# Kernel optimization log

Measured on AMD Instinct MI355X. Metric: run time of the kernel, lower is better.

The kernel has to match this reference:

```python
import jax, jax.numpy as jnp
from jax import lax
import numpy as np

B, T, I, H, C = 32, 256, 128, 128, 100


def setup_inputs() -> dict:
    key = jax.random.key(0)
    ks = jax.random.split(key, 9)
    s = 1.0 / np.sqrt(H)  # PyTorch LSTMCell init range
    inp = {
        "x": jax.random.normal(ks[0], (B, T, I), dtype=jnp.float32),
        "w_ih": jax.random.uniform(ks[1], (4 * H, I), jnp.float32, -s, s),
        "b_ih": jax.random.uniform(ks[2], (4 * H,), jnp.float32, -s, s),
        "w_hh": jax.random.uniform(ks[3], (4 * H, H), jnp.float32, -s, s),
        "b_hh": jax.random.uniform(ks[4], (4 * H,), jnp.float32, -s, s),
        # attention params: normal(mean=0, std=0.01) per the source
        "w1": 0.01 * jax.random.normal(ks[5], (2 * H, H), dtype=jnp.float32),
        "w2": 0.01 * jax.random.normal(ks[6], (H, 1), dtype=jnp.float32),
        "w_fc": jax.random.uniform(ks[7], (C, H), jnp.float32, -s, s),
        "b_fc": jax.random.uniform(ks[8], (C,), jnp.float32, -s, s),
    }
    return inp


def _forward(x, w_ih, b_ih, w_hh, b_hh, w1, w2, w_fc, b_fc):
    Bv, Tv, _ = x.shape
    Hv = w_hh.shape[1]
    h0 = jnp.zeros((Bv, Hv), x.dtype)
    c0 = jnp.zeros((Bv, Hv), x.dtype)
    # memory buffer: slot 0 holds the initial zero hidden state (as in the
    # torch code, h_old starts as h_t=0); slots 1..T filled as we go.
    # Unwritten (future) slots are zero, so their attn contribution
    # attn_w * h_old is exactly zero -> no mask needed, matching the
    # growing-memory semantics of the original loop.
    mem0 = jnp.zeros((Bv, Tv + 1, Hv), x.dtype)
    attn0 = jnp.zeros((Bv, Hv), x.dtype)

    def step(carry, inp):
        h, c, mem, _ = carry
        x_t, i = inp
        # PyTorch LSTMCell: gate order i, f, g, o
        gates = x_t @ w_ih.T + b_ih + h @ w_hh.T + b_hh
        ig, fg, gg, og = jnp.split(gates, 4, axis=-1)
        c = jax.nn.sigmoid(fg) * c + jax.nn.sigmoid(ig) * jnp.tanh(gg)
        h = jax.nn.sigmoid(og) * jnp.tanh(c)
        # additive attention scores over the memory (NO softmax in source)
        h_rep = jnp.broadcast_to(h[:, None, :], mem.shape)  # [B, T+1, H]
        cat = jnp.concatenate([h_rep, mem], axis=-1)        # [B, T+1, 2H]
        s = jnp.tanh(cat @ w1) @ w2                          # [B, T+1, 1]
        attn_c = jnp.sum(s * mem, axis=1)                    # [B, H]
        mem = mem.at[:, i + 1, :].set(h)  # append h_t to memory
        return (h, c, mem, attn_c), None

    xs = (jnp.transpose(x, (1, 0, 2)), jnp.arange(Tv))
    (h, c, mem, attn_c), _ = lax.scan(step, (h0, c0, mem0, attn0), xs)
    return (h + attn_c) @ w_fc.T + b_fc


def reference(x, w_ih, b_ih, w_hh, b_hh, w1, w2, w_fc, b_fc):
    return _forward(x, w_ih, b_ih, w_hh, b_hh, w1, w2, w_fc, b_fc)
```

## Files before the change

kernel.cpp:

```cpp
#include <hip/hip_runtime.h>
#include <hip/hip_bf16.h>


#define Bsz 32
#define Tsz 256
#define Isz 128
#define Hsz 128
#define Csz 100
#define G4H 512

typedef short v8s __attribute__((ext_vector_type(8)));
typedef float v4fa __attribute__((ext_vector_type(4)));
typedef float v2f __attribute__((ext_vector_type(2)));

__device__ __forceinline__ v2f mk2(float a, float b) { v2f r; r.x = a; r.y = b; return r; }
__device__ __forceinline__ float quad_rsum(float x) {
    int t = __builtin_amdgcn_update_dpp(0, __float_as_int(x), 0xB1, 0xF, 0xF, true);
    x += __int_as_float(t);
    t = __builtin_amdgcn_update_dpp(0, __float_as_int(x), 0x4E, 0xF, 0xF, true);
    x += __int_as_float(t);
    return x;
}
__device__ __forceinline__ float rcpf(float x) { return __builtin_amdgcn_rcpf(x); }
__device__ __forceinline__ float ex2(float x) { return __builtin_amdgcn_exp2f(x); }
__device__ __forceinline__ float sigm_n(float x) {
    return rcpf(1.0f + ex2(-1.442695041f * x));
}
__device__ __forceinline__ float tanh_n(float x) {
    return fmaf(-2.0f, rcpf(1.0f + ex2(2.885390082f * x)), 1.0f);
}
__device__ __forceinline__ short bf16_bits(float x) {
    __hip_bfloat16 h = __float2bfloat16(x);
    return *reinterpret_cast<short*>(&h);
}
__device__ __forceinline__ float bf16_val(float x) {
    return __bfloat162float(__float2bfloat16(x));
}

__global__ __launch_bounds__(256) void prep_kernel(
    const float* __restrict__ w_ih, const float* __restrict__ b_ih,
    const float* __restrict__ w_hh, const float* __restrict__ b_hh,
    const float* __restrict__ w1,
    __hip_bfloat16* __restrict__ W2ih, __hip_bfloat16* __restrict__ W2v,
    float* __restrict__ whh_pk, float* __restrict__ bias,
    float* __restrict__ attn_c) {
    int idx = blockIdx.x * blockDim.x + threadIdx.x;
    if (idx < G4H * Isz) {
        int n = idx >> 7;
        int k = idx & 127;
        float x = w_ih[idx];
        __hip_bfloat16 hi = __float2bfloat16(x);
        __hip_bfloat16 lo = __float2bfloat16(x - __bfloat162float(hi));
        W2ih[(size_t)n * 384 + k] = hi;
        W2ih[(size_t)n * 384 + 128 + k] = lo;
        W2ih[(size_t)n * 384 + 256 + k] = hi;

        int j4  = idx & 3;
        int q   = (idx >> 2) & 3;
        int d   = (idx >> 4) & 127;
        int gi  = (idx >> 11) & 3;
        int kk4 = (idx >> 13) & 7;
        whh_pk[idx] = w_hh[(size_t)((gi << 7) + d) * 128 + (q << 5) + (kk4 << 2) + j4];
    }
    if (idx < Hsz * Hsz) {
        int n = idx >> 7;
        int k = idx & 127;
        float x = w1[(size_t)(128 + k) * Hsz + n];
        __hip_bfloat16 hi = __float2bfloat16(x);
        __hip_bfloat16 lo = __float2bfloat16(x - __bfloat162float(hi));
        W2v[(size_t)n * 384 + k] = hi;
        W2v[(size_t)n * 384 + 128 + k] = lo;
        W2v[(size_t)n * 384 + 256 + k] = hi;
    }
    if (idx < G4H) bias[idx] = b_ih[idx] + b_hh[idx];
    if (idx < Bsz * Hsz) attn_c[idx] = 0.0f;
}

__global__ __launch_bounds__(256) void gemm_mfma_f32a(
    const float* __restrict__ A, const __hip_bfloat16* __restrict__ W2,
    const float* __restrict__ bias, float* __restrict__ C, int M, int N) {
    const int tid = threadIdx.x;
    const int w = tid >> 6, lane = tid & 63;
    const int m0 = blockIdx.y * 64 + (w & 1) * 32;
    const int n0 = blockIdx.x * 64 + (w >> 1) * 32;
    const int r = lane & 15, quad = lane >> 4;

    v8s Ahi[2][4], Alo[2][4];
    #pragma unroll
    for (int i = 0; i < 2; ++i)
        #pragma unroll
        for (int cb = 0; cb < 4; ++cb) {
            const float* src = A + (size_t)(m0 + 16 * i + r) * Isz + cb * 32 + quad * 8;
            float4 f0 = *(const float4*)src;
            float4 f1 = *(const float4*)(src + 4);
            float f[8] = {f0.x, f0.y, f0.z, f0.w, f1.x, f1.y, f1.z, f1.w};
            v8s hi, lo;
            #pragma unroll
            for (int e = 0; e < 8; ++e) {
                float hv = bf16_val(f[e]);
                hi[e] = bf16_bits(f[e]);
                lo[e] = bf16_bits(f[e] - hv);
            }
            Ahi[i][cb] = hi;
            Alo[i][cb] = lo;
        }

    v4fa acc[2][2] = {};
    const short* Wb = (const short*)W2;
    #pragma unroll
    for (int ks = 0; ks < 12; ++ks) {
        int cb = ks & 3;
        v8s a0 = (ks >= 8) ? Alo[0][cb] : Ahi[0][cb];
        v8s a1 = (ks >= 8) ? Alo[1][cb] : Ahi[1][cb];
        int kb = ks * 32 + quad * 8;
        v8s b0 = *(const v8s*)(Wb + (size_t)(n0 + r) * 384 + kb);
        v8s b1 = *(const v8s*)(Wb + (size_t)(n0 + 16 + r) * 384 + kb);
        acc[0][0] = __builtin_amdgcn_mfma_f32_16x16x32_bf16(a0, b0, acc[0][0], 0, 0, 0);
        acc[0][1] = __builtin_amdgcn_mfma_f32_16x16x32_bf16(a0, b1, acc[0][1], 0, 0, 0);
        acc[1][0] = __builtin_amdgcn_mfma_f32_16x16x32_bf16(a1, b0, acc[1][0], 0, 0, 0);
        acc[1][1] = __builtin_amdgcn_mfma_f32_16x16x32_bf16(a1, b1, acc[1][1], 0, 0, 0);
    }
    #pragma unroll
    for (int i = 0; i < 2; ++i)
        #pragma unroll
        for (int j = 0; j < 2; ++j) {
            int cn = n0 + 16 * j + r;
            float bb = bias ? bias[cn] : 0.0f;
            #pragma unroll
            for (int rr = 0; rr < 4; ++rr) {
                int row = m0 + 16 * i + quad * 4 + rr;
                C[(size_t)row * N + cn] = acc[i][j][rr] + bb;
            }
        }
}

#define HPAD(k) ((k) + 8 * ((k) >> 5))

__global__ __launch_bounds__(512, 2) void lstm_seq(
    const float* __restrict__ G, const float* __restrict__ whh_pk,
    float* __restrict__ H_all) {
    const int b = blockIdx.x;
    const int tid = threadIdx.x;
    const int d = tid >> 2;
    const int q = tid & 3;

    __shared__ float h_s[2][160];

    v2f w2v[4][16];
    {
        const float4* wp = (const float4*)whh_pk;
        #pragma unroll
        for (int kk4 = 0; kk4 < 8; ++kk4)
            #pragma unroll
            for (int gi = 0; gi < 4; ++gi) {
                float4 v = wp[((kk4 * 4 + gi) * 128 + d) * 4 + q];
                w2v[gi][kk4 * 2]     = mk2(v.x, v.y);
                w2v[gi][kk4 * 2 + 1] = mk2(v.z, v.w);
            }
    }

    if (tid < 320) ((float*)h_s)[tid] = 0.0f;
    float c = 0.0f;
    __syncthreads();

    const float* Gq = G + (size_t)b * Tsz * G4H + q * 128 + d;
    float* Hst = H_all + (size_t)b * Tsz * Hsz + d;

    float gval = Gq[0];
    int cur = 0;
    for (int t = 0; t < Tsz; ++t) {
        const int tn = (t < Tsz - 1) ? t + 1 : t;
        float ngval = Gq[(size_t)tn * G4H];

        v2f accA[4], accB[4];
        #pragma unroll
        for (int gi = 0; gi < 4; ++gi) {
            accA[gi] = mk2(q == gi ? gval : 0.f, 0.f);
            accB[gi] = mk2(0.f, 0.f);
        }
        const float4* hb4 = (const float4*)&h_s[cur][q * 40];
        #pragma unroll
        for (int kk4 = 0; kk4 < 8; ++kk4) {
            float4 h4 = hb4[kk4];
            v2f hA = mk2(h4.x, h4.y);
            v2f hB = mk2(h4.z, h4.w);
            accA[0] = __builtin_elementwise_fma(hA, w2v[0][2 * kk4], accA[0]);
            accA[1] = __builtin_elementwise_fma(hA, w2v[1][2 * kk4], accA[1]);
            accA[2] = __builtin_elementwise_fma(hA, w2v[2][2 * kk4], accA[2]);
            accA[3] = __builtin_elementwise_fma(hA, w2v[3][2 * kk4], accA[3]);
            accB[0] = __builtin_elementwise_fma(hB, w2v[0][2 * kk4 + 1], accB[0]);
            accB[1] = __builtin_elementwise_fma(hB, w2v[1][2 * kk4 + 1], accB[1]);
            accB[2] = __builtin_elementwise_fma(hB, w2v[2][2 * kk4 + 1], accB[2]);
            accB[3] = __builtin_elementwise_fma(hB, w2v[3][2 * kk4 + 1], accB[3]);
        }
        float a0 = quad_rsum(accA[0].x + accA[0].y + accB[0].x + accB[0].y);
        float a1 = quad_rsum(accA[1].x + accA[1].y + accB[1].x + accB[1].y);
        float a2 = quad_rsum(accA[2].x + accA[2].y + accB[2].x + accB[2].y);
        float a3 = quad_rsum(accA[3].x + accA[3].y + accB[3].x + accB[3].y);

        float iv = sigm_n(a0);
        float fv = sigm_n(a1);
        float gv = tanh_n(a2);
        float ov = sigm_n(a3);
        c = fmaf(fv, c, iv * gv);
        float h = ov * tanh_n(c);

        if (q == 0) {
            h_s[cur ^ 1][HPAD(d)] = h;
            Hst[(size_t)t * Hsz] = h;
        }
        gval = ngval;
        __builtin_amdgcn_sched_barrier(0);
        asm volatile("s_waitcnt lgkmcnt(0)" ::: "memory");
        __builtin_amdgcn_s_barrier();
        __builtin_amdgcn_sched_barrier(0);
        cur ^= 1;
    }
}

__global__ __launch_bounds__(256) void kv_scores(
    const float* __restrict__ H_all, const __hip_bfloat16* __restrict__ W2v,
    const float* __restrict__ w1, const float* __restrict__ w2,
    float* __restrict__ attn_c) {
    const int b = blockIdx.x >> 2, jt = blockIdx.x & 3;
    const int tid = threadIdx.x;
    __shared__ float kv_s[64][132];
    __shared__ float hT[Hsz];
    __shared__ float q_s[Hsz];
    __shared__ float w2s[Hsz];
    __shared__ float s_s[64];
    __shared__ float part[2][Hsz];

    const float* Hb = H_all + (size_t)b * Tsz * Hsz;

    if (tid < Hsz) {
        hT[tid] = Hb[255 * Hsz + tid];
        w2s[tid] = w2[tid];
    }

    {
        const int w = tid >> 6, lane = tid & 63;
        const int m0 = (w & 1) * 32;
        const int n0 = (w >> 1) * 32;
        const int r = lane & 15, quad = lane >> 4;
        const float* Abase = Hb + (size_t)(jt * 64) * Hsz;

        v8s Ahi[2][4], Alo[2][4];
        #pragma unroll
        for (int i = 0; i < 2; ++i)
            #pragma unroll
            for (int cb = 0; cb < 4; ++cb) {
                const float* src = Abase + (size_t)(m0 + 16 * i + r) * Hsz + cb * 32 + quad * 8;
                float4 f0 = *(const float4*)src;
                float4 f1 = *(const float4*)(src + 4);
                float f[8] = {f0.x, f0.y, f0.z, f0.w, f1.x, f1.y, f1.z, f1.w};
                v8s hi, lo;
                #pragma unroll
                for (int e = 0; e < 8; ++e) {
                    float hv = bf16_val(f[e]);
                    hi[e] = bf16_bits(f[e]);
                    lo[e] = bf16_bits(f[e] - hv);
                }
                Ahi[i][cb] = hi;
                Alo[i][cb] = lo;
            }

        v4fa acc[2][2][2] = {};
        const short* Wb = (const short*)W2v;
        #pragma unroll
        for (int ks = 0; ks < 12; ++ks) {
            int cb = ks & 3;
            v8s a0 = (ks >= 8) ? Alo[0][cb] : Ahi[0][cb];
            v8s a1 = (ks >= 8) ? Alo[1][cb] : Ahi[1][cb];
            int kb = ks * 32 + quad * 8;
            #pragma unroll
            for (int nh = 0; nh < 2; ++nh) {
                int nn = nh * 64 + n0;
                v8s b0 = *(const v8s*)(Wb + (size_t)(nn + r) * 384 + kb);
                v8s b1 = *(const v8s*)(Wb + (size_t)(nn + 16 + r) * 384 + kb);
                acc[nh][0][0] = __builtin_amdgcn_mfma_f32_16x16x32_bf16(a0, b0, acc[nh][0][0], 0, 0, 0);
                acc[nh][0][1] = __builtin_amdgcn_mfma_f32_16x16x32_bf16(a0, b1, acc[nh][0][1], 0, 0, 0);
                acc[nh][1][0] = __builtin_amdgcn_mfma_f32_16x16x32_bf16(a1, b0, acc[nh][1][0], 0, 0, 0);
                acc[nh][1][1] = __builtin_amdgcn_mfma_f32_16x16x32_bf16(a1, b1, acc[nh][1][1], 0, 0, 0);
            }
        }
        #pragma unroll
        for (int nh = 0; nh < 2; ++nh)
            #pragma unroll
            for (int i = 0; i < 2; ++i)
                #pragma unroll
                for (int j = 0; j < 2; ++j)
                    #pragma unroll
                    for (int rr = 0; rr < 4; ++rr)
                        kv_s[m0 + 16 * i + quad * 4 + rr][nh * 64 + n0 + 16 * j + r] =
                            acc[nh][i][j][rr];
    }
    __syncthreads();

    if (tid < Hsz) {
        float acc = 0.f;
        #pragma unroll 8
        for (int k = 0; k < Hsz; ++k) acc = fmaf(hT[k], w1[k * Hsz + tid], acc);
        q_s[tid] = acc;
    }
    __syncthreads();

    const int jl = tid >> 2, ql = tid & 3;
    const int j = jt * 64 + jl;
    float p = 0.f;
    if (j < 255) {
        #pragma unroll 8
        for (int kk = 0; kk < 32; ++kk) {
            int k = ql * 32 + ((kk + ql) & 31);
            p = fmaf(tanh_n(q_s[k] + kv_s[jl][k]), w2s[k], p);
        }
    }
    p = quad_rsum(p);
    if (ql == 0) s_s[jl] = (j < 255) ? p : 0.0f;
    __syncthreads();

    {
        const int dd = tid & 127, half = tid >> 7;
        float acc = 0.f;
        #pragma unroll 4
        for (int u = 0; u < 32; ++u) {
            int lj = half * 32 + u;
            int jj = jt * 64 + lj;
            if (jj < 255) acc = fmaf(s_s[lj], Hb[(size_t)jj * Hsz + dd], acc);
        }
        part[half][dd] = acc;
    }
    __syncthreads();
    if (tid < Hsz) atomicAdd(&attn_c[b * Hsz + tid], part[0][tid] + part[1][tid]);
}

__global__ __launch_bounds__(256) void fc_out(
    const float* __restrict__ H_all, const float* __restrict__ attn_c,
    const float* __restrict__ w_fc, const float* __restrict__ b_fc,
    float* __restrict__ out) {
    const int b = blockIdx.x, tid = threadIdx.x;
    __shared__ float r_s[Hsz];
    if (tid < Hsz)
        r_s[tid] = H_all[(size_t)b * Tsz * Hsz + 255 * Hsz + tid] + attn_c[b * Hsz + tid];
    __syncthreads();
    const int o = tid >> 1, half = tid & 1;
    float acc = 0.f;
    if (o < Csz) {
        const float* wr = w_fc + (size_t)o * Hsz + half * 64;
        const float* rr = r_s + half * 64;
        #pragma unroll 8
        for (int k = 0; k < 64; ++k) acc = fmaf(rr[k], wr[k], acc);
    }
    acc += __shfl_xor(acc, 1);
    if (half == 0 && o < Csz) out[b * Csz + o] = acc + b_fc[o];
}

extern "C" void kernel_launch(void* const* d_in, const int* in_sizes, int n_in,
                              void* d_out, int out_size, void* d_ws, size_t ws_size,
                              hipStream_t stream) {
    const float* x    = (const float*)d_in[0];
    const float* w_ih = (const float*)d_in[1];
    const float* b_ih = (const float*)d_in[2];
    const float* w_hh = (const float*)d_in[3];
    const float* b_hh = (const float*)d_in[4];
    const float* w1   = (const float*)d_in[5];
    const float* w2   = (const float*)d_in[6];
    const float* w_fc = (const float*)d_in[7];
    const float* b_fc = (const float*)d_in[8];

    float* ws = (float*)d_ws;
    float* whh_pk = ws;
    float* bias   = whh_pk + 65536;
    float* attn_c = bias + 512;
    __hip_bfloat16* W2ih = (__hip_bfloat16*)(attn_c + 4096);
    __hip_bfloat16* W2v  = (__hip_bfloat16*)(attn_c + 4096 + 98304);
    float* G      = attn_c + 4096 + 98304 + 24576;
    float* H_all  = G + 4194304;

    prep_kernel<<<256, 256, 0, stream>>>(w_ih, b_ih, w_hh, b_hh, w1,
                                         W2ih, W2v, whh_pk, bias, attn_c);

    dim3 gG(G4H / 64, (Bsz * Tsz) / 64);
    gemm_mfma_f32a<<<gG, 256, 0, stream>>>(x, W2ih, bias, G, Bsz * Tsz, G4H);

    lstm_seq<<<Bsz, 512, 0, stream>>>(G, whh_pk, H_all);

    kv_scores<<<Bsz * 4, 256, 0, stream>>>(H_all, W2v, w1, w2, attn_c);

    fc_out<<<Bsz, 256, 0, stream>>>(H_all, attn_c, w_fc, b_fc, (float*)d_out);
}
```

Before: 340.9 us.

## Split LSTM recurrent dot product across eight lanes with 1024-thread blocks

```diff
diff --git a/kernel.cpp b/kernel.cpp
--- a/kernel.cpp
+++ b/kernel.cpp
@@ -11,9 +11,21 @@
 
 typedef short v8s __attribute__((ext_vector_type(8)));
 typedef float v4fa __attribute__((ext_vector_type(4)));
-typedef float v2f __attribute__((ext_vector_type(2)));
-
-__device__ __forceinline__ v2f mk2(float a, float b) { v2f r; r.x = a; r.y = b; return r; }
+
+__device__ __forceinline__ float2 pk_fma(float2 a, float2 b, float2 c) {
+    float2 d;
+    asm("v_pk_fma_f32 %0, %1, %2, %3" : "=v"(d) : "v"(a), "v"(b), "v"(c));
+    return d;
+}
+__device__ __forceinline__ float oct_rsum(float x) {
+    int t = __builtin_amdgcn_update_dpp(0, __float_as_int(x), 0xB1, 0xF, 0xF, true);
+    x += __int_as_float(t);
+    t = __builtin_amdgcn_update_dpp(0, __float_as_int(x), 0x4E, 0xF, 0xF, true);
+    x += __int_as_float(t);
+    t = __builtin_amdgcn_update_dpp(0, __float_as_int(x), 0x141, 0xF, 0xF, true);
+    x += __int_as_float(t);
+    return x;
+}
 __device__ __forceinline__ float quad_rsum(float x) {
     int t = __builtin_amdgcn_update_dpp(0, __float_as_int(x), 0xB1, 0xF, 0xF, true);
     x += __int_as_float(t);
@@ -55,12 +67,14 @@
         W2ih[(size_t)n * 384 + 128 + k] = lo;
         W2ih[(size_t)n * 384 + 256 + k] = hi;
 
-        int j4  = idx & 3;
-        int q   = (idx >> 2) & 3;
-        int d   = (idx >> 4) & 127;
-        int gi  = (idx >> 11) & 3;
-        int kk4 = (idx >> 13) & 7;
-        whh_pk[idx] = w_hh[(size_t)((gi << 7) + d) * 128 + (q << 5) + (kk4 << 2) + j4];
+        int c   = idx & 3;
+        int t   = (idx >> 2) & 1023;
+        int f   = idx >> 12;
+        int d   = t >> 3;
+        int q   = t & 7;
+        int gi  = f & 3;
+        int j4  = f >> 2;
+        whh_pk[idx] = w_hh[(size_t)((gi << 7) + d) * 128 + (q << 4) + (j4 << 2) + c];
     }
     if (idx < Hsz * Hsz) {
         int n = idx >> 7;
@@ -136,34 +150,33 @@
 
 #define HPAD(k) ((k) + 8 * ((k) >> 5))
 
-__global__ __launch_bounds__(512, 2) void lstm_seq(
+__global__ __launch_bounds__(1024, 4) void lstm_seq(
     const float* __restrict__ G, const float* __restrict__ whh_pk,
     float* __restrict__ H_all) {
     const int b = blockIdx.x;
     const int tid = threadIdx.x;
-    const int d = tid >> 2;
-    const int q = tid & 3;
+    const int d = tid >> 3;
+    const int q = tid & 7;
 
     __shared__ float h_s[2][160];
 
-    v2f w2v[4][16];
+    float2 w2v[4][8];
     {
         const float4* wp = (const float4*)whh_pk;
         #pragma unroll
-        for (int kk4 = 0; kk4 < 8; ++kk4)
-            #pragma unroll
-            for (int gi = 0; gi < 4; ++gi) {
-                float4 v = wp[((kk4 * 4 + gi) * 128 + d) * 4 + q];
-                w2v[gi][kk4 * 2]     = mk2(v.x, v.y);
-                w2v[gi][kk4 * 2 + 1] = mk2(v.z, v.w);
-            }
+        for (int f = 0; f < 16; ++f) {
+            float4 v = wp[f * 1024 + tid];
+            int gi = f & 3, j4 = f >> 2;
+            w2v[gi][j4 * 2]     = make_float2(v.x, v.y);
+            w2v[gi][j4 * 2 + 1] = make_float2(v.z, v.w);
+        }
     }
 
     if (tid < 320) ((float*)h_s)[tid] = 0.0f;
     float c = 0.0f;
     __syncthreads();
 
-    const float* Gq = G + (size_t)b * Tsz * G4H + q * 128 + d;
+    const float* Gq = G + (size_t)b * Tsz * G4H + (q & 3) * 128 + d;
     float* Hst = H_all + (size_t)b * Tsz * Hsz + d;
 
     float gval = Gq[0];
@@ -172,31 +185,31 @@
         const int tn = (t < Tsz - 1) ? t + 1 : t;
         float ngval = Gq[(size_t)tn * G4H];
 
-        v2f accA[4], accB[4];
+        float2 accA[4], accB[4];
         #pragma unroll
         for (int gi = 0; gi < 4; ++gi) {
-            accA[gi] = mk2(q == gi ? gval : 0.f, 0.f);
-            accB[gi] = mk2(0.f, 0.f);
-        }
-        const float4* hb4 = (const float4*)&h_s[cur][q * 40];
-        #pragma unroll
-        for (int kk4 = 0; kk4 < 8; ++kk4) {
-            float4 h4 = hb4[kk4];
-            v2f hA = mk2(h4.x, h4.y);
-            v2f hB = mk2(h4.z, h4.w);
-            accA[0] = __builtin_elementwise_fma(hA, w2v[0][2 * kk4], accA[0]);
-            accA[1] = __builtin_elementwise_fma(hA, w2v[1][2 * kk4], accA[1]);
-            accA[2] = __builtin_elementwise_fma(hA, w2v[2][2 * kk4], accA[2]);
-            accA[3] = __builtin_elementwise_fma(hA, w2v[3][2 * kk4], accA[3]);
-            accB[0] = __builtin_elementwise_fma(hB, w2v[0][2 * kk4 + 1], accB[0]);
-            accB[1] = __builtin_elementwise_fma(hB, w2v[1][2 * kk4 + 1], accB[1]);
-            accB[2] = __builtin_elementwise_fma(hB, w2v[2][2 * kk4 + 1], accB[2]);
-            accB[3] = __builtin_elementwise_fma(hB, w2v[3][2 * kk4 + 1], accB[3]);
-        }
-        float a0 = quad_rsum(accA[0].x + accA[0].y + accB[0].x + accB[0].y);
-        float a1 = quad_rsum(accA[1].x + accA[1].y + accB[1].x + accB[1].y);
-        float a2 = quad_rsum(accA[2].x + accA[2].y + accB[2].x + accB[2].y);
-        float a3 = quad_rsum(accA[3].x + accA[3].y + accB[3].x + accB[3].y);
+            accA[gi] = make_float2(q == gi ? gval : 0.f, 0.f);
+            accB[gi] = make_float2(0.f, 0.f);
+        }
+        const float4* hb4 = (const float4*)&h_s[cur][q * 16 + 8 * (q >> 1)];
+        #pragma unroll
+        for (int j4 = 0; j4 < 4; ++j4) {
+            float4 h4 = hb4[j4];
+            float2 hA = make_float2(h4.x, h4.y);
+            float2 hB = make_float2(h4.z, h4.w);
+            accA[0] = pk_fma(hA, w2v[0][2 * j4], accA[0]);
+            accA[1] = pk_fma(hA, w2v[1][2 * j4], accA[1]);
+            accA[2] = pk_fma(hA, w2v[2][2 * j4], accA[2]);
+            accA[3] = pk_fma(hA, w2v[3][2 * j4], accA[3]);
+            accB[0] = pk_fma(hB, w2v[0][2 * j4 + 1], accB[0]);
+            accB[1] = pk_fma(hB, w2v[1][2 * j4 + 1], accB[1]);
+            accB[2] = pk_fma(hB, w2v[2][2 * j4 + 1], accB[2]);
+            accB[3] = pk_fma(hB, w2v[3][2 * j4 + 1], accB[3]);
+        }
+        float a0 = oct_rsum(accA[0].x + accA[0].y + accB[0].x + accB[0].y);
+        float a1 = oct_rsum(accA[1].x + accA[1].y + accB[1].x + accB[1].y);
+        float a2 = oct_rsum(accA[2].x + accA[2].y + accB[2].x + accB[2].y);
+        float a3 = oct_rsum(accA[3].x + accA[3].y + accB[3].x + accB[3].y);
 
         float iv = sigm_n(a0);
         float fv = sigm_n(a1);
@@ -383,7 +396,7 @@
     dim3 gG(G4H / 64, (Bsz * Tsz) / 64);
     gemm_mfma_f32a<<<gG, 256, 0, stream>>>(x, W2ih, bias, G, Bsz * Tsz, G4H);
 
-    lstm_seq<<<Bsz, 512, 0, stream>>>(G, whh_pk, H_all);
+    lstm_seq<<<Bsz, 1024, 0, stream>>>(G, whh_pk, H_all);
 
     kv_scores<<<Bsz * 4, 256, 0, stream>>>(H_all, W2v, w1, w2, attn_c);
 
```

Result: slower. 378.8 us (+11.1%).

## Compute LSTM recurrent matvec with split-bf16 MFMA instead of packed FP32 FMAs

Applied to the files above, without the earlier changes.

```diff
diff --git a/kernel.cpp b/kernel.cpp
--- a/kernel.cpp
+++ b/kernel.cpp
@@ -11,9 +11,7 @@
 
 typedef short v8s __attribute__((ext_vector_type(8)));
 typedef float v4fa __attribute__((ext_vector_type(4)));
-typedef float v2f __attribute__((ext_vector_type(2)));
-
-__device__ __forceinline__ v2f mk2(float a, float b) { v2f r; r.x = a; r.y = b; return r; }
+
 __device__ __forceinline__ float quad_rsum(float x) {
     int t = __builtin_amdgcn_update_dpp(0, __float_as_int(x), 0xB1, 0xF, 0xF, true);
     x += __int_as_float(t);
@@ -41,26 +39,29 @@
     const float* __restrict__ w_ih, const float* __restrict__ b_ih,
     const float* __restrict__ w_hh, const float* __restrict__ b_hh,
     const float* __restrict__ w1,
-    __hip_bfloat16* __restrict__ W2ih, __hip_bfloat16* __restrict__ W2v,
-    float* __restrict__ whh_pk, float* __restrict__ bias,
-    float* __restrict__ attn_c) {
+    __hip_bfloat16* __restrict__ W2ih, __hip_bfloat16* __restrict__ W2hh,
+    __hip_bfloat16* __restrict__ W2v,
+    float* __restrict__ bias, float* __restrict__ attn_c) {
     int idx = blockIdx.x * blockDim.x + threadIdx.x;
     if (idx < G4H * Isz) {
         int n = idx >> 7;
         int k = idx & 127;
-        float x = w_ih[idx];
-        __hip_bfloat16 hi = __float2bfloat16(x);
-        __hip_bfloat16 lo = __float2bfloat16(x - __bfloat162float(hi));
-        W2ih[(size_t)n * 384 + k] = hi;
-        W2ih[(size_t)n * 384 + 128 + k] = lo;
-        W2ih[(size_t)n * 384 + 256 + k] = hi;
-
-        int j4  = idx & 3;
-        int q   = (idx >> 2) & 3;
-        int d   = (idx >> 4) & 127;
-        int gi  = (idx >> 11) & 3;
-        int kk4 = (idx >> 13) & 7;
-        whh_pk[idx] = w_hh[(size_t)((gi << 7) + d) * 128 + (q << 5) + (kk4 << 2) + j4];
+        {
+            float x = w_ih[idx];
+            __hip_bfloat16 hi = __float2bfloat16(x);
+            __hip_bfloat16 lo = __float2bfloat16(x - __bfloat162float(hi));
+            W2ih[(size_t)n * 384 + k] = hi;
+            W2ih[(size_t)n * 384 + 128 + k] = lo;
+            W2ih[(size_t)n * 384 + 256 + k] = hi;
+        }
+        {
+            float x = w_hh[idx];
+            __hip_bfloat16 hi = __float2bfloat16(x);
+            __hip_bfloat16 lo = __float2bfloat16(x - __bfloat162float(hi));
+            W2hh[(size_t)n * 384 + k] = hi;
+            W2hh[(size_t)n * 384 + 128 + k] = lo;
+            W2hh[(size_t)n * 384 + 256 + k] = hi;
+        }
     }
     if (idx < Hsz * Hsz) {
         int n = idx >> 7;
@@ -134,82 +135,91 @@
         }
 }
 
-#define HPAD(k) ((k) + 8 * ((k) >> 5))
-
 __global__ __launch_bounds__(512, 2) void lstm_seq(
-    const float* __restrict__ G, const float* __restrict__ whh_pk,
+    const float* __restrict__ G, const __hip_bfloat16* __restrict__ W2hh,
     float* __restrict__ H_all) {
     const int b = blockIdx.x;
     const int tid = threadIdx.x;
-    const int d = tid >> 2;
-    const int q = tid & 3;
-
-    __shared__ float h_s[2][160];
-
-    v2f w2v[4][16];
+    const int w = tid >> 6;
+    const int lane = tid & 63;
+    const int r = lane & 15;
+    const int quad = lane >> 4;
+
+    __shared__ alignas(16) short hhi[2][128];
+    __shared__ alignas(16) short hlo[2][128];
+
+    v8s wb[4][8];
     {
-        const float4* wp = (const float4*)whh_pk;
-        #pragma unroll
-        for (int kk4 = 0; kk4 < 8; ++kk4)
-            #pragma unroll
-            for (int gi = 0; gi < 4; ++gi) {
-                float4 v = wp[((kk4 * 4 + gi) * 128 + d) * 4 + q];
-                w2v[gi][kk4 * 2]     = mk2(v.x, v.y);
-                w2v[gi][kk4 * 2 + 1] = mk2(v.z, v.w);
+        const short* Wb = (const short*)W2hh;
+        #pragma unroll
+        for (int g = 0; g < 4; ++g)
+            #pragma unroll
+            for (int j = 0; j < 8; ++j) {
+                int n = g * 128 + w * 16 + r;
+                wb[g][j] = *(const v8s*)(Wb + (size_t)n * 384 + j * 32 + quad * 8);
             }
     }
 
-    if (tid < 320) ((float*)h_s)[tid] = 0.0f;
+    if (tid < 128) {
+        hhi[0][tid] = 0; hlo[0][tid] = 0;
+        hhi[1][tid] = 0; hlo[1][tid] = 0;
+    }
     float c = 0.0f;
-    __syncthreads();
-
-    const float* Gq = G + (size_t)b * Tsz * G4H + q * 128 + d;
-    float* Hst = H_all + (size_t)b * Tsz * Hsz + d;
-
-    float gval = Gq[0];
+
+    const float* Gq = G + (size_t)b * Tsz * G4H + w * 16 + r;
+    float* Hst = H_all + (size_t)b * Tsz * Hsz + w * 16 + r;
+
+    float gv0 = 0.f, gv1 = 0.f, gv2 = 0.f, gv3 = 0.f;
+    if (quad == 0) {
+        gv0 = Gq[0]; gv1 = Gq[128]; gv2 = Gq[256]; gv3 = Gq[384];
+    }
+    __syncthreads();
+
     int cur = 0;
     for (int t = 0; t < Tsz; ++t) {
+        v8s ahi[4], alo[4];
+        #pragma unroll
+        for (int cb = 0; cb < 4; ++cb) {
+            ahi[cb] = *(const v8s*)&hhi[cur][cb * 32 + quad * 8];
+            alo[cb] = *(const v8s*)&hlo[cur][cb * 32 + quad * 8];
+        }
+
         const int tn = (t < Tsz - 1) ? t + 1 : t;
-        float ngval = Gq[(size_t)tn * G4H];
-
-        v2f accA[4], accB[4];
-        #pragma unroll
-        for (int gi = 0; gi < 4; ++gi) {
-            accA[gi] = mk2(q == gi ? gval : 0.f, 0.f);
-            accB[gi] = mk2(0.f, 0.f);
-        }
-        const float4* hb4 = (const float4*)&h_s[cur][q * 40];
-        #pragma unroll
-        for (int kk4 = 0; kk4 < 8; ++kk4) {
-            float4 h4 = hb4[kk4];
-            v2f hA = mk2(h4.x, h4.y);
-            v2f hB = mk2(h4.z, h4.w);
-            accA[0] = __builtin_elementwise_fma(hA, w2v[0][2 * kk4], accA[0]);
-            accA[1] = __builtin_elementwise_fma(hA, w2v[1][2 * kk4], accA[1]);
-            accA[2] = __builtin_elementwise_fma(hA, w2v[2][2 * kk4], accA[2]);
-            accA[3] = __builtin_elementwise_fma(hA, w2v[3][2 * kk4], accA[3]);
-            accB[0] = __builtin_elementwise_fma(hB, w2v[0][2 * kk4 + 1], accB[0]);
-            accB[1] = __builtin_elementwise_fma(hB, w2v[1][2 * kk4 + 1], accB[1]);
-            accB[2] = __builtin_elementwise_fma(hB, w2v[2][2 * kk4 + 1], accB[2]);
-            accB[3] = __builtin_elementwise_fma(hB, w2v[3][2 * kk4 + 1], accB[3]);
-        }
-        float a0 = quad_rsum(accA[0].x + accA[0].y + accB[0].x + accB[0].y);
-        float a1 = quad_rsum(accA[1].x + accA[1].y + accB[1].x + accB[1].y);
-        float a2 = quad_rsum(accA[2].x + accA[2].y + accB[2].x + accB[2].y);
-        float a3 = quad_rsum(accA[3].x + accA[3].y + accB[3].x + accB[3].y);
-
-        float iv = sigm_n(a0);
-        float fv = sigm_n(a1);
-        float gv = tanh_n(a2);
-        float ov = sigm_n(a3);
-        c = fmaf(fv, c, iv * gv);
+        float gn0 = 0.f, gn1 = 0.f, gn2 = 0.f, gn3 = 0.f;
+        if (quad == 0) {
+            const float* Gt = Gq + (size_t)tn * G4H;
+            gn0 = Gt[0]; gn1 = Gt[128]; gn2 = Gt[256]; gn3 = Gt[384];
+        }
+
+        v4fa acc0 = {}, acc1 = {}, acc2 = {}, acc3 = {};
+        if (quad == 0) { acc0[0] = gv0; acc1[0] = gv1; acc2[0] = gv2; acc3[0] = gv3; }
+
+        #pragma unroll
+        for (int ks = 0; ks < 12; ++ks) {
+            const int cb = ks & 3;
+            const int j = (ks < 8) ? ks : ks - 8;
+            v8s a = (ks >= 8) ? alo[cb] : ahi[cb];
+            acc0 = __builtin_amdgcn_mfma_f32_16x16x32_bf16(a, wb[0][j], acc0, 0, 0, 0);
+            acc1 = __builtin_amdgcn_mfma_f32_16x16x32_bf16(a, wb[1][j], acc1, 0, 0, 0);
+            acc2 = __builtin_amdgcn_mfma_f32_16x16x32_bf16(a, wb[2][j], acc2, 0, 0, 0);
+            acc3 = __builtin_amdgcn_mfma_f32_16x16x32_bf16(a, wb[3][j], acc3, 0, 0, 0);
+        }
+
+        float iv = sigm_n(acc0[0]);
+        float fv = sigm_n(acc1[0]);
+        float gg = tanh_n(acc2[0]);
+        float ov = sigm_n(acc3[0]);
+        c = fmaf(fv, c, iv * gg);
         float h = ov * tanh_n(c);
 
-        if (q == 0) {
-            h_s[cur ^ 1][HPAD(d)] = h;
+        if (quad == 0) {
+            float hv = bf16_val(h);
+            hhi[cur ^ 1][w * 16 + r] = bf16_bits(h);
+            hlo[cur ^ 1][w * 16 + r] = bf16_bits(h - hv);
             Hst[(size_t)t * Hsz] = h;
         }
-        gval = ngval;
+        gv0 = gn0; gv1 = gn1; gv2 = gn2; gv3 = gn3;
+
         __builtin_amdgcn_sched_barrier(0);
         asm volatile("s_waitcnt lgkmcnt(0)" ::: "memory");
         __builtin_amdgcn_s_barrier();
@@ -369,21 +379,21 @@
     const float* b_fc = (const float*)d_in[8];
 
     float* ws = (float*)d_ws;
-    float* whh_pk = ws;
-    float* bias   = whh_pk + 65536;
+    float* bias   = ws;
     float* attn_c = bias + 512;
     __hip_bfloat16* W2ih = (__hip_bfloat16*)(attn_c + 4096);
-    __hip_bfloat16* W2v  = (__hip_bfloat16*)(attn_c + 4096 + 98304);
-    float* G      = attn_c + 4096 + 98304 + 24576;
+    __hip_bfloat16* W2hh = (__hip_bfloat16*)(attn_c + 4096 + 98304);
+    __hip_bfloat16* W2v  = (__hip_bfloat16*)(attn_c + 4096 + 196608);
+    float* G      = attn_c + 4096 + 196608 + 24576;
     float* H_all  = G + 4194304;
 
     prep_kernel<<<256, 256, 0, stream>>>(w_ih, b_ih, w_hh, b_hh, w1,
-                                         W2ih, W2v, whh_pk, bias, attn_c);
+                                         W2ih, W2hh, W2v, bias, attn_c);
 
     dim3 gG(G4H / 64, (Bsz * Tsz) / 64);
     gemm_mfma_f32a<<<gG, 256, 0, stream>>>(x, W2ih, bias, G, Bsz * Tsz, G4H);
 
-    lstm_seq<<<Bsz, 512, 0, stream>>>(G, whh_pk, H_all);
+    lstm_seq<<<Bsz, 512, 0, stream>>>(G, W2hh, H_all);
 
     kv_scores<<<Bsz * 4, 256, 0, stream>>>(H_all, W2v, w1, w2, attn_c);
 
```

Result: slower. 444.0 us (+30.2%).
